# Kernel optimization log

Hardware: AMD Instinct MI355X
Metric: run time of the kernel (lower is better)

The kernel has to match this reference:

```python
import jax, jax.numpy as jnp
import numpy as np
from jax import lax

IMG, P, C, D, H, L, B = 256, 16, 3, 768, 12, 8, 2
G = IMG // P            # 16
N = G * G               # 256 patches
FF = 2048               # hard-coded FFN hidden dim in ViTBlockWithCCAttention
DH = D // H
EPS = 1e-5


def setup_inputs() -> dict:
    key = jax.random.key(0)
    ks = jax.random.split(key, 24)
    s = 0.02
    rn = lambda k, shp: jax.random.normal(k, shp, jnp.float32) * s
    inp = {
        "x": jax.random.normal(ks[0], (B, C, IMG, IMG), jnp.float32),
        "patch_w": rn(ks[1], (D, C * P * P)),
        "patch_b": rn(ks[2], (D,)),
        "pos_embed": rn(ks[3], (1, N, D)),
        # per-layer stacked params (shared nn.MultiheadAttention per block)
        "in_proj_w": rn(ks[4], (L, 3 * D, D)),
        "in_proj_b": rn(ks[5], (L, 3 * D)),
        "out_w": rn(ks[6], (L, D, D)),
        "out_b": rn(ks[7], (L, D)),
        "ln1_g": jnp.ones((L, D), jnp.float32),
        "ln1_b": jnp.zeros((L, D), jnp.float32),
        "ln2_g": jnp.ones((L, D), jnp.float32),
        "ln2_b": jnp.zeros((L, D), jnp.float32),
        "ffn_w1": rn(ks[8], (L, FF, D)),
        "ffn_b1": rn(ks[9], (L, FF)),
        "ffn_w2": rn(ks[10], (L, D, FF)),
        "ffn_b2": rn(ks[11], (L, D)),
        "edge_w": rn(ks[12], (D, 1)),
        "edge_b": rn(ks[13], (D,)),
        "conv1_w": rn(ks[14], (256, D, 3, 3)),
        "conv1_b": rn(ks[15], (256,)),
        "conv2_w": rn(ks[16], (1, 256, 1, 1)),
        "conv2_b": rn(ks[17], (1,)),
    }
    return inp


def _ln(z, g, b):
    m = z.mean(-1, keepdims=True)
    v = ((z - m) ** 2).mean(-1, keepdims=True)
    return (z - m) / jnp.sqrt(v + EPS) * g + b


def _mha(z, wi, bi, wo, bo):
    # z: (M, S, D). Returns out (M,S,D) and head-averaged attn weights (M,S,S)
    M, S, _ = z.shape
    qkv = z @ wi.T + bi
    q, k, v = jnp.split(qkv, 3, axis=-1)
    sp = lambda t: t.reshape(M, S, H, DH).transpose(0, 2, 1, 3)  # (M,H,S,dh)
    q, k, v = sp(q), sp(k), sp(v)
    a = jax.nn.softmax(jnp.einsum('mhqd,mhkd->mhqk', q, k) / np.sqrt(DH).astype(np.float32), axis=-1)
    o = jnp.einsum('mhqk,mhkd->mhqd', a, v).transpose(0, 2, 1, 3).reshape(M, S, D)
    return o @ wo.T + bo, a.mean(1)


def reference(x, patch_w, patch_b, pos_embed, in_proj_w, in_proj_b, out_w, out_b,
              ln1_g, ln1_b, ln2_g, ln2_b, ffn_w1, ffn_b1, ffn_w2, ffn_b2,
              edge_w, edge_b, conv1_w, conv1_b, conv2_w, conv2_b):
    Bc = x.shape[0]
    # patch embedding: unfold -> (B, N, C*P*P) -> linear
    patches = x.reshape(Bc, C, G, P, G, P).transpose(0, 2, 4, 1, 3, 5).reshape(Bc, N, C * P * P)
    h = patches @ patch_w.T + patch_b + pos_embed

    edge_sum = jnp.zeros((Bc, N, D), h.dtype)
    for i in range(L):
        xl = _ln(h, ln1_g[i], ln1_b[i])
        x2d = xl.reshape(Bc, G, G, D)
        # rows: sequences along height, one per column
        row_x = x2d.transpose(0, 2, 1, 3).reshape(Bc * G, G, D)
        row_out, row_a = _mha(row_x, in_proj_w[i], in_proj_b[i], out_w[i], out_b[i])
        # cols: sequences along width, one per row
        col_x = x2d.reshape(Bc * G, G, D)
        col_out, col_a = _mha(col_x, in_proj_w[i], in_proj_b[i], out_w[i], out_b[i])
        attn_out = (row_out.reshape(Bc, G, G, D).transpose(0, 2, 1, 3)
                    + col_out.reshape(Bc, G, G, D)).reshape(Bc, N, D)
        h = h + attn_out
        z = _ln(h, ln2_g[i], ln2_b[i])
        h = h + jax.nn.relu(z @ ffn_w1[i].T + ffn_b1[i]) @ ffn_w2[i].T + ffn_b2[i]
        # attention-divergence edge tokens (query-averaged attn maps)
        div = jnp.abs(row_a.mean(1) - col_a.mean(1)).reshape(Bc, N, 1)
        edge_sum = edge_sum + (div @ edge_w.T + edge_b)
    h = h + edge_sum / L

    feat = h.transpose(0, 2, 1).reshape(Bc, D, G, G)
    feat = jax.image.resize(feat, (Bc, D, IMG, IMG), method="bilinear")  # align_corners=False
    dn = ("NCHW", "OIHW", "NCHW")
    y = lax.conv_general_dilated(feat, conv1_w, (1, 1), "SAME", dimension_numbers=dn)
    y = jax.nn.relu(y + conv1_b[None, :, None, None])
    y = lax.conv_general_dilated(y, conv2_w, (1, 1), "SAME", dimension_numbers=dn)
    return y + conv2_b[None, :, None, None]
```

## Files before the change

kernel.cpp:

```cpp
#include <hip/hip_runtime.h>
#include <hip/hip_bf16.h>
#include <math.h>

#define BB 2
#define CIN 3
#define IMGS 256
#define PS 16
#define GG 16
#define NN 256
#define DIM 768
#define NH 12
#define NL 8
#define FFD 2048
#define LNEPS 1e-5f

typedef __attribute__((ext_vector_type(8))) short bf16x8;
typedef __attribute__((ext_vector_type(4))) float f32x4;

#define MB     1
#define MB2    2
#define MPOS   4
#define MRELU  8
#define MRES   16
#define MOBF16 32
#define MAS2   64
#define MBF32  128
#define MLNA   256
#define MAIM2  512

__device__ inline unsigned short bc(float f) {
    return __builtin_bit_cast(unsigned short, __float2bfloat16(f));
}

__device__ inline void gload16(const unsigned short* g, unsigned short* l) {
    __builtin_amdgcn_global_load_lds((const __attribute__((address_space(1))) void*)g,
                                     (__attribute__((address_space(3))) void*)l, 16, 0, 0);
}

template<int MODE, int BN>
__global__ __launch_bounds__(256) void gemm_bf16(
    const void* __restrict__ Av, const void* __restrict__ A2v, const void* __restrict__ Bv,
    const float* __restrict__ bias, const float* __restrict__ pos,
    const float2* __restrict__ stats, const float* __restrict__ lng,
    const float* __restrict__ lnb,
    float* __restrict__ C, unsigned short* __restrict__ C16,
    int M, int N, int K, int zdiv,
    long long sAo, long long sBi, long long sCo, long long sCi)
{
    constexpr int NI = BN / 32;
    int z = blockIdx.y;
    int zo = z / zdiv, zi = z % zdiv;
    const unsigned short* A16 = (const unsigned short*)Av + (size_t)zo * sAo;
    const float* Af  = (const float*)Av  + (size_t)zo * sAo;
    const float* Af2 = (const float*)A2v + (size_t)zo * sAo;
    const unsigned short* B16 = (const unsigned short*)Bv + (size_t)zi * sBi;
    const float* Bf  = (const float*)Bv  + (size_t)zi * sBi;
    long long coff = (long long)zo * sCo + (long long)zi * sCi;

    int NBY = M >> 5;
    int nbysh = 31 - __builtin_clz(NBY);
    int id = blockIdx.x;
    int qch = gridDim.x >> 3;
    int wgid = (id & 7) * qch + (id >> 3);
    int bx = wgid >> nbysh, by = wgid & (NBY - 1);
    int bm = by * 32, bn = bx * BN;

    __shared__ __align__(16) unsigned short As[2][2048], Bs[2][BN * 64];
    int tid = threadIdx.x;
    int lane = tid & 63, wave = tid >> 6;
    int wr = wave >> 1, wc = wave & 1;
    int sA = tid;
    int srowA = sA >> 3, schkA = (sA & 7) ^ (srowA & 7);

    f32x4 acc[NI] = {};
    f32x4 rA0, rA1, rA20, rA21, rB[NI][2], gv0, gv1, bv0, bv1;
    float2 strow;

    auto gstageA = [&](int b, int kt) {
        gload16(A16 + (size_t)(bm + srowA) * K + kt * 64 + schkA * 8, &As[b][sA * 8]);
    };
    auto gstageB = [&](int b, int kt) {
        #pragma unroll
        for (int i = 0; i < NI; ++i) {
            int s = tid + i * 256;
            int row = s >> 3, chk = (s & 7) ^ (row & 7);
            gload16(B16 + (size_t)(bn + row) * K + kt * 64 + chk * 8, &Bs[b][s * 8]);
        }
    };
    auto ldA = [&](int kt) {
        int k0 = kt * 64 + schkA * 8;
        if constexpr (MODE & MAIM2) {
            int m = bm + srowA;
            int bq = m >> 8, n = m & 255, gy = n >> 4, gx = n & 15;
            int c = k0 >> 8, rem = k0 & 255, py = rem >> 4, px = rem & 15;
            const float* src = Af + (((size_t)(bq * CIN + c) * IMGS + gy * PS + py) << 8)
                             + gx * PS + px;
            rA0 = *(const f32x4*)(src);
            rA1 = *(const f32x4*)(src + 4);
        } else {
            size_t off = (size_t)(bm + srowA) * K + k0;
            rA0 = *(const f32x4*)(Af + off);
            rA1 = *(const f32x4*)(Af + off + 4);
            if constexpr (MODE & MAS2) {
                rA20 = *(const f32x4*)(Af2 + off);
                rA21 = *(const f32x4*)(Af2 + off + 4);
            }
            if constexpr (MODE & MLNA) {
                strow = stats[bm + srowA];
                gv0 = *(const f32x4*)(lng + k0); gv1 = *(const f32x4*)(lng + k0 + 4);
                bv0 = *(const f32x4*)(lnb + k0); bv1 = *(const f32x4*)(lnb + k0 + 4);
            }
        }
    };
    auto ldB = [&](int kt) {
        #pragma unroll
        for (int i = 0; i < NI; ++i) {
            int s = tid + i * 256;
            int row = s >> 3, chk = (s & 7) ^ (row & 7);
            size_t off = (size_t)(bn + row) * K + kt * 64 + chk * 8;
            rB[i][0] = *(const f32x4*)(Bf + off);
            rB[i][1] = *(const f32x4*)(Bf + off + 4);
        }
    };
    auto wrA = [&](int b) {
        bf16x8 v;
        #pragma unroll
        for (int j = 0; j < 4; ++j) {
            float x0 = rA0[j], x1 = rA1[j];
            if constexpr (MODE & MAS2) { x0 += rA20[j]; x1 += rA21[j]; }
            if constexpr (MODE & MLNA) {
                x0 = (x0 - strow.x) * strow.y * gv0[j] + bv0[j];
                x1 = (x1 - strow.x) * strow.y * gv1[j] + bv1[j];
            }
            v[j] = (short)bc(x0); v[4 + j] = (short)bc(x1);
        }
        *(bf16x8*)(&As[b][sA * 8]) = v;
    };
    auto wrB = [&](int b) {
        #pragma unroll
        for (int i = 0; i < NI; ++i) {
            int s = tid + i * 256;
            bf16x8 v;
            #pragma unroll
            for (int j = 0; j < 4; ++j) {
                v[j] = (short)bc(rB[i][0][j]); v[4 + j] = (short)bc(rB[i][1][j]);
            }
            *(bf16x8*)(&Bs[b][s * 8]) = v;
        }
    };
    constexpr bool regA = (MODE & (MAS2 | MLNA | MAIM2)) != 0;
    auto compute = [&](int b) {
        const unsigned short* Ab = As[b];
        const unsigned short* Bb = Bs[b];
        int rl = lane & 15, kh = lane >> 4;
        #pragma unroll
        for (int ks = 0; ks < 2; ++ks) {
            int kc = ks * 4 + kh;
            int ar = 16 * wr + rl;
            bf16x8 af = *(const bf16x8*)(Ab + ar * 64 + (kc ^ (ar & 7)) * 8);
            #pragma unroll
            for (int ni = 0; ni < NI; ++ni) {
                int br = 16 * NI * wc + 16 * ni + rl;
                bf16x8 bf = *(const bf16x8*)(Bb + br * 64 + (kc ^ (br & 7)) * 8);
                acc[ni] = __builtin_amdgcn_mfma_f32_16x16x32_bf16(af, bf, acc[ni], 0, 0, 0);
            }
        }
    };

    int nt = K >> 6;
    if constexpr (!regA) gstageA(0, 0); else { ldA(0); wrA(0); }
    if constexpr (!(MODE & MBF32)) gstageB(0, 0); else { ldB(0); wrB(0); }
    __syncthreads();
    int buf = 0;
    for (int t = 0; t < nt; ++t) {
        if (t + 1 < nt) {
            if constexpr (!regA) gstageA(buf ^ 1, t + 1); else ldA(t + 1);
            if constexpr (!(MODE & MBF32)) gstageB(buf ^ 1, t + 1); else ldB(t + 1);
        }
        compute(buf);
        if (t + 1 < nt) {
            if constexpr (regA) wrA(buf ^ 1);
            if constexpr (MODE & MBF32) wrB(buf ^ 1);
        }
        __syncthreads();
        buf ^= 1;
    }

    #pragma unroll
    for (int ni = 0; ni < NI; ++ni) {
        #pragma unroll
        for (int r = 0; r < 4; ++r) {
            int row = bm + 16 * wr + (lane >> 4) * 4 + r;
            int col = bn + 16 * NI * wc + 16 * ni + (lane & 15);
            float v = acc[ni][r];
            if (MODE & (MB | MB2)) v += bias[col] * ((MODE & MB2) ? 2.f : 1.f);
            if (MODE & MPOS) v += pos[(size_t)(row & (NN - 1)) * N + col];
            if (MODE & MRELU) v = fmaxf(v, 0.f);
            long long ci = coff + (long long)row * N + col;
            if (MODE & MOBF16) C16[ci] = bc(v);
            else if (MODE & MRES) C[ci] += v;
            else C[ci] = v;
        }
    }
}

__global__ void wct_kernel(const float* __restrict__ w, unsigned short* __restrict__ Wct)
{
    int idx = blockIdx.x * 256 + threadIdx.x;
    int c = idx % DIM;
    int t = idx / DIM;
    int oc = t & 255;
    int dydx = t >> 8;
    int dy = dydx / 3, dx = dydx % 3;
    Wct[idx] = bc(w[((size_t)(oc * DIM + c) * 3 + dy) * 3 + dx]);
}

__global__ __launch_bounds__(256) void lnstat_kernel(const float* __restrict__ X,
                                                     float2* __restrict__ st)
{
    int row = blockIdx.x * 4 + (threadIdx.x >> 6);
    int lane = threadIdx.x & 63;
    const float* xp = X + (size_t)row * DIM + lane * 4;
    float s = 0.f, s2 = 0.f;
    #pragma unroll
    for (int seg = 0; seg < 3; ++seg) {
        f32x4 v = *(const f32x4*)(xp + seg * 256);
        s += v[0] + v[1] + v[2] + v[3];
        s2 += v[0] * v[0] + v[1] * v[1] + v[2] * v[2] + v[3] * v[3];
    }
    #pragma unroll
    for (int off = 32; off > 0; off >>= 1) {
        s  += __shfl_xor(s, off);
        s2 += __shfl_xor(s2, off);
    }
    if (lane == 0) {
        float mean = s * (1.f / DIM);
        float var = s2 * (1.f / DIM) - mean * mean;
        st[row] = make_float2(mean, rsqrtf(var + LNEPS));
    }
}

__global__ __launch_bounds__(256) void attn_kernel(
    const float* __restrict__ qkv, float* __restrict__ orow,
    float* __restrict__ ocol, float* __restrict__ amh)
{
    int b = blockIdx.x >> 4, g = blockIdx.x & 15;
    int type = blockIdx.y;
    int hh = blockIdx.z;
    int tid = threadIdx.x;
    __shared__ float qs[16][68], ks[16][68], vs[16][68], as_[16][17];
    {
        int sr = tid >> 4, dq = tid & 15;
        int n = (type == 0) ? (sr * GG + g) : (g * GG + sr);
        const float* base = qkv + (size_t)(b * NN + n) * (3 * DIM) + hh * 64 + dq * 4;
        float4 qv = *(const float4*)(base);
        float4 kv = *(const float4*)(base + DIM);
        float4 vv = *(const float4*)(base + 2 * DIM);
        *(float4*)&qs[sr][dq * 4] = qv;
        *(float4*)&ks[sr][dq * 4] = kv;
        *(float4*)&vs[sr][dq * 4] = vv;
    }
    __syncthreads();
    int s = tid >> 4, t = tid & 15;
    float sc = 0.f;
    #pragma unroll
    for (int d = 0; d < 64; ++d) sc += qs[s][d] * ks[t][d];
    sc *= 0.125f;
    float mx = sc;
    #pragma unroll
    for (int off = 1; off < 16; off <<= 1) mx = fmaxf(mx, __shfl_xor(mx, off, 16));
    float p = __expf(sc - mx);
    float sum = p;
    #pragma unroll
    for (int off = 1; off < 16; off <<= 1) sum += __shfl_xor(sum, off, 16);
    as_[s][t] = p / sum;
    __syncthreads();
    if (tid < 16) {
        float a = 0.f;
        #pragma unroll
        for (int ss = 0; ss < 16; ++ss) a += as_[ss][tid];
        amh[((size_t)(type * BB + b) * NN + g * GG + tid) * NH + hh] = a;
    }
    int s2 = tid >> 4, dg = (tid & 15) * 4;
    float o0 = 0, o1 = 0, o2 = 0, o3 = 0;
    #pragma unroll
    for (int t2 = 0; t2 < 16; ++t2) {
        float a2 = as_[s2][t2];
        o0 += a2 * vs[t2][dg];
        o1 += a2 * vs[t2][dg + 1];
        o2 += a2 * vs[t2][dg + 2];
        o3 += a2 * vs[t2][dg + 3];
    }
    int n2 = (type == 0) ? (s2 * GG + g) : (g * GG + s2);
    float* op = ((type == 0) ? orow : ocol) + (size_t)(b * NN + n2) * DIM + hh * 64 + dg;
    *(float4*)op = make_float4(o0, o1, o2, o3);
}

__global__ __launch_bounds__(256) void hfin_kernel(
    const float* __restrict__ h, const float* __restrict__ amh,
    const float* __restrict__ ew, const float* __restrict__ eb,
    unsigned short* __restrict__ hf)
{
    int m = blockIdx.x;
    int b = m >> 8, n = m & 255;
    int tid = threadIdx.x;
    __shared__ float divs;
    if (tid < 8) {
        const float* base = amh + (size_t)tid * 12288 + (size_t)b * 3072 + n * 12;
        float rs = 0.f, cs = 0.f;
        #pragma unroll
        for (int hh = 0; hh < NH; ++hh) {
            rs += base[hh];
            cs += base[6144 + hh];
        }
        float d = fabsf(rs - cs);
        d += __shfl_xor(d, 1);
        d += __shfl_xor(d, 2);
        d += __shfl_xor(d, 4);
        if (tid == 0) divs = d * (1.f / (NH * GG)) * (1.f / NL);
    }
    __syncthreads();
    float dv = divs;
    const float* hp = h + (size_t)m * DIM;
    unsigned short* yp = hf + (size_t)m * DIM;
    #pragma unroll
    for (int seg = 0; seg < 3; ++seg) {
        int d0 = tid + seg * 256;
        yp[d0] = bc(hp[d0] + dv * ew[d0] + eb[d0]);
    }
}

__global__ __launch_bounds__(256) void s_kernel(const float* __restrict__ P, float* __restrict__ S)
{
    int bdy = blockIdx.y;
    int b = bdy / 3, dy = bdy % 3;
    int ocg = blockIdx.x;
    __shared__ float Pl[3][4][16][17];
    int tid = threadIdx.x;
    #pragma unroll
    for (int l = 0; l < 12; ++l) {
        int e = l * 256 + tid;
        int dx = e >> 10, rem = e & 1023;
        int oc = rem >> 8, pix = rem & 255;
        int i = pix >> 4, j = pix & 15;
        Pl[dx][oc][j][i] =
            P[(((size_t)b * 9 + dy * 3 + dx) * 256 + ocg * 4 + oc) * 256 + pix];
    }
    __syncthreads();
    int xq = tid >> 6, oc = (tid >> 4) & 3, i = tid & 15;
    for (int xx = 0; xx < 64; ++xx) {
        int x = xq * 64 + xx;
        float acc = 0.f;
        #pragma unroll
        for (int dx = 0; dx < 3; ++dx) {
            int u = x + dx - 1;
            float p = (u + 0.5f) * 0.0625f - 0.5f;
            float fl = floorf(p);
            float f = p - fl;
            int j0 = (int)fl;
            int ja = j0 < 0 ? 0 : j0;
            int jb = (j0 + 1 > 15) ? 15 : (j0 + 1);
            bool valid = (u >= 0) && (u <= 255);
            float w0 = valid ? 1.f - f : 0.f;
            float w1 = valid ? f : 0.f;
            acc += w0 * Pl[dx][oc][ja][i] + w1 * Pl[dx][oc][jb][i];
        }
        S[(((size_t)(b * 256 + x) * 3 + dy) * 256 + ocg * 4 + oc) * 16 + i] = acc;
    }
}

__global__ __launch_bounds__(256) void out_kernel(
    const float* __restrict__ S, const float* __restrict__ b1,
    const float* __restrict__ w2, const float* __restrict__ b2p,
    float* __restrict__ out)
{
    int b = blockIdx.x >> 8, x = blockIdx.x & 255;
    __shared__ float Sl[12288];
    const float* Sp = S + (size_t)(b * 256 + x) * 12288;
    for (int l = threadIdx.x; l < 12288; l += 256) Sl[l] = Sp[l];
    __syncthreads();
    int y = threadIdx.x;
    float wy[3][2];
    int iy[3][2];
    #pragma unroll
    for (int dy = 0; dy < 3; ++dy) {
        int v = y + dy - 1;
        if (v < 0 || v > 255) {
            wy[dy][0] = wy[dy][1] = 0.f;
            iy[dy][0] = iy[dy][1] = 0;
        } else {
            float pp = (v + 0.5f) * 0.0625f - 0.5f;
            float fl = floorf(pp);
            float f = pp - fl;
            int i0 = (int)fl;
            iy[dy][0] = i0 < 0 ? 0 : i0;
            iy[dy][1] = (i0 + 1 > 15) ? 15 : (i0 + 1);
            wy[dy][0] = 1.f - f;
            wy[dy][1] = f;
        }
    }
    float acc = 0.f;
    for (int oc = 0; oc < 256; ++oc) {
        float sv = 0.f;
        #pragma unroll
        for (int dy = 0; dy < 3; ++dy)
            sv += wy[dy][0] * Sl[dy * 4096 + oc * 16 + iy[dy][0]]
                + wy[dy][1] * Sl[dy * 4096 + oc * 16 + iy[dy][1]];
        sv += b1[oc];
        acc += fmaxf(sv, 0.f) * w2[oc];
    }
    out[(size_t)b * 65536 + y * 256 + x] = acc + b2p[0];
}

extern "C" void kernel_launch(void* const* d_in, const int* in_sizes, int n_in,
                              void* d_out, int out_size, void* d_ws, size_t ws_size,
                              hipStream_t stream)
{
    const float* x         = (const float*)d_in[0];
    const float* patch_w   = (const float*)d_in[1];
    const float* patch_b   = (const float*)d_in[2];
    const float* pos_embed = (const float*)d_in[3];
    const float* in_proj_w = (const float*)d_in[4];
    const float* in_proj_b = (const float*)d_in[5];
    const float* out_w     = (const float*)d_in[6];
    const float* out_b     = (const float*)d_in[7];
    const float* ln1_g     = (const float*)d_in[8];
    const float* ln1_b     = (const float*)d_in[9];
    const float* ln2_g     = (const float*)d_in[10];
    const float* ln2_b     = (const float*)d_in[11];
    const float* ffn_w1    = (const float*)d_in[12];
    const float* ffn_b1    = (const float*)d_in[13];
    const float* ffn_w2    = (const float*)d_in[14];
    const float* ffn_b2    = (const float*)d_in[15];
    const float* edge_w    = (const float*)d_in[16];
    const float* edge_b    = (const float*)d_in[17];
    const float* conv1_w   = (const float*)d_in[18];
    const float* conv1_b   = (const float*)d_in[19];
    const float* conv2_w   = (const float*)d_in[20];
    const float* conv2_b   = (const float*)d_in[21];
    float* out = (float*)d_out;
    float* ws = (float*)d_ws;

    float* h      = ws;
    float* qkv    = h + 393216;
    float* orow   = qkv + 1179648;
    float* ocol   = orow + 393216;
    float* Pb     = ocol + 393216;
    float* Sb     = Pb + 1179648;
    float* amh    = Sb + 6291456;
    float2* stats = (float2*)(amh + 98304);
    unsigned short* hid16  = (unsigned short*)(amh + 98304 + 1024);
    unsigned short* hfin16 = hid16 + 1048576;
    unsigned short* Wct16  = hfin16 + 393216;

    wct_kernel<<<dim3(6912), 256, 0, stream>>>(conv1_w, Wct16);
    gemm_bf16<MB | MPOS | MAIM2 | MBF32, 32><<<dim3(24 * 16), 256, 0, stream>>>(
        x, nullptr, patch_w, patch_b, pos_embed, nullptr, nullptr, nullptr,
        h, nullptr, 512, 768, 768, 1, 0, 0, 0, 0);

    for (int l = 0; l < NL; ++l) {
        lnstat_kernel<<<dim3(128), 256, 0, stream>>>(h, stats);
        gemm_bf16<MB | MLNA | MBF32, 64><<<dim3(36 * 16), 256, 0, stream>>>(
            h, nullptr, in_proj_w + (size_t)l * 1769472,
            in_proj_b + (size_t)l * 2304, nullptr, stats,
            ln1_g + l * DIM, ln1_b + l * DIM, qkv, nullptr,
            512, 2304, 768, 1, 0, 0, 0, 0);
        attn_kernel<<<dim3(BB * GG, 2, NH), 256, 0, stream>>>(
            qkv, orow, ocol, amh + (size_t)l * 12288);
        gemm_bf16<MB2 | MRES | MAS2 | MBF32, 32><<<dim3(24 * 16), 256, 0, stream>>>(
            orow, ocol, out_w + (size_t)l * 589824,
            out_b + (size_t)l * DIM, nullptr, nullptr, nullptr, nullptr,
            h, nullptr, 512, 768, 768, 1, 0, 0, 0, 0);
        lnstat_kernel<<<dim3(128), 256, 0, stream>>>(h, stats);
        gemm_bf16<MB | MRELU | MOBF16 | MLNA | MBF32, 64><<<dim3(32 * 16), 256, 0, stream>>>(
            h, nullptr, ffn_w1 + (size_t)l * 1572864,
            ffn_b1 + (size_t)l * FFD, nullptr, stats,
            ln2_g + l * DIM, ln2_b + l * DIM, nullptr, hid16,
            512, 2048, 768, 1, 0, 0, 0, 0);
        gemm_bf16<MB | MRES | MBF32, 32><<<dim3(24 * 16), 256, 0, stream>>>(
            hid16, nullptr, ffn_w2 + (size_t)l * 1572864,
            ffn_b2 + (size_t)l * DIM, nullptr, nullptr, nullptr, nullptr,
            h, nullptr, 512, 768, 2048, 1, 0, 0, 0, 0);
    }

    hfin_kernel<<<dim3(512), 256, 0, stream>>>(h, amh, edge_w, edge_b, hfin16);
    gemm_bf16<0, 32><<<dim3(8 * 8, 18), 256, 0, stream>>>(
        Wct16, nullptr, hfin16, nullptr, nullptr, nullptr, nullptr, nullptr,
        Pb, nullptr, 256, 256, 768,
        2, 196608LL, 196608LL, 65536LL, 589824LL);
    s_kernel<<<dim3(64, 6), 256, 0, stream>>>(Pb, Sb);
    out_kernel<<<dim3(512), 256, 0, stream>>>(Sb, conv1_b, conv2_w, conv2_b, out);
}
```

Baseline: 663.7 us.

## Fuse LayerNorm stats into GEMM prologue and store conv intermediate as bf16

Removes the separate lnstat kernel launches: each LN-consuming GEMM block computes mean and rstd for its 32 rows into shared memory before the main loop. The intermediate S buffer between s_kernel and out_kernel is stored in bf16 instead of fp32, halving that traffic, and out_kernel unpacks it with vectorized loads. This trades 16 launches for redundant per-block stat computation (every column block recomputes the same rows) and adds bf16 rounding error on the conv intermediate.

```diff
diff --git a/kernel.cpp b/kernel.cpp
--- a/kernel.cpp
+++ b/kernel.cpp
@@ -15,6 +15,7 @@
 #define LNEPS 1e-5f
 
 typedef __attribute__((ext_vector_type(8))) short bf16x8;
+typedef __attribute__((ext_vector_type(8))) unsigned short u16x8;
 typedef __attribute__((ext_vector_type(4))) float f32x4;
 
 #define MB     1
@@ -31,6 +32,10 @@
 __device__ inline unsigned short bc(float f) {
     return __builtin_bit_cast(unsigned short, __float2bfloat16(f));
 }
+__device__ inline float fbc(unsigned short u) {
+    unsigned int x = ((unsigned int)u) << 16;
+    return __builtin_bit_cast(float, x);
+}
 
 __device__ inline void gload16(const unsigned short* g, unsigned short* l) {
     __builtin_amdgcn_global_load_lds((const __attribute__((address_space(1))) void*)g,
@@ -41,8 +46,7 @@
 __global__ __launch_bounds__(256) void gemm_bf16(
     const void* __restrict__ Av, const void* __restrict__ A2v, const void* __restrict__ Bv,
     const float* __restrict__ bias, const float* __restrict__ pos,
-    const float2* __restrict__ stats, const float* __restrict__ lng,
-    const float* __restrict__ lnb,
+    const float* __restrict__ lng, const float* __restrict__ lnb,
     float* __restrict__ C, unsigned short* __restrict__ C16,
     int M, int N, int K, int zdiv,
     long long sAo, long long sBi, long long sCo, long long sCi)
@@ -66,11 +70,35 @@
     int bm = by * 32, bn = bx * BN;
 
     __shared__ __align__(16) unsigned short As[2][2048], Bs[2][BN * 64];
+    __shared__ float2 sstat[32];
     int tid = threadIdx.x;
     int lane = tid & 63, wave = tid >> 6;
     int wr = wave >> 1, wc = wave & 1;
     int sA = tid;
     int srowA = sA >> 3, schkA = (sA & 7) ^ (srowA & 7);
+
+    if constexpr (MODE & MLNA) {
+        int r = tid >> 3, sub = tid & 7;
+        const float* rp = Af + (size_t)(bm + r) * K + sub * 96;
+        float s = 0.f, s2 = 0.f;
+        #pragma unroll
+        for (int i = 0; i < 24; ++i) {
+            f32x4 v = *(const f32x4*)(rp + i * 4);
+            s  += v[0] + v[1] + v[2] + v[3];
+            s2 += v[0]*v[0] + v[1]*v[1] + v[2]*v[2] + v[3]*v[3];
+        }
+        #pragma unroll
+        for (int m2 = 1; m2 < 8; m2 <<= 1) {
+            s  += __shfl_xor(s, m2);
+            s2 += __shfl_xor(s2, m2);
+        }
+        if (sub == 0) {
+            float mean = s * (1.f / DIM);
+            float var = s2 * (1.f / DIM) - mean * mean;
+            sstat[r] = make_float2(mean, rsqrtf(var + LNEPS));
+        }
+        __syncthreads();
+    }
 
     f32x4 acc[NI] = {};
     f32x4 rA0, rA1, rA20, rA21, rB[NI][2], gv0, gv1, bv0, bv1;
@@ -106,7 +134,7 @@
                 rA21 = *(const f32x4*)(Af2 + off + 4);
             }
             if constexpr (MODE & MLNA) {
-                strow = stats[bm + srowA];
+                strow = sstat[srowA];
                 gv0 = *(const f32x4*)(lng + k0); gv1 = *(const f32x4*)(lng + k0 + 4);
                 bv0 = *(const f32x4*)(lnb + k0); bv1 = *(const f32x4*)(lnb + k0 + 4);
             }
@@ -213,31 +241,6 @@
     int dydx = t >> 8;
     int dy = dydx / 3, dx = dydx % 3;
     Wct[idx] = bc(w[((size_t)(oc * DIM + c) * 3 + dy) * 3 + dx]);
-}
-
-__global__ __launch_bounds__(256) void lnstat_kernel(const float* __restrict__ X,
-                                                     float2* __restrict__ st)
-{
-    int row = blockIdx.x * 4 + (threadIdx.x >> 6);
-    int lane = threadIdx.x & 63;
-    const float* xp = X + (size_t)row * DIM + lane * 4;
-    float s = 0.f, s2 = 0.f;
-    #pragma unroll
-    for (int seg = 0; seg < 3; ++seg) {
-        f32x4 v = *(const f32x4*)(xp + seg * 256);
-        s += v[0] + v[1] + v[2] + v[3];
-        s2 += v[0] * v[0] + v[1] * v[1] + v[2] * v[2] + v[3] * v[3];
-    }
-    #pragma unroll
-    for (int off = 32; off > 0; off >>= 1) {
-        s  += __shfl_xor(s, off);
-        s2 += __shfl_xor(s2, off);
-    }
-    if (lane == 0) {
-        float mean = s * (1.f / DIM);
-        float var = s2 * (1.f / DIM) - mean * mean;
-        st[row] = make_float2(mean, rsqrtf(var + LNEPS));
-    }
 }
 
 __global__ __launch_bounds__(256) void attn_kernel(
@@ -330,7 +333,8 @@
     }
 }
 
-__global__ __launch_bounds__(256) void s_kernel(const float* __restrict__ P, float* __restrict__ S)
+__global__ __launch_bounds__(256) void s_kernel(const float* __restrict__ P,
+                                               unsigned short* __restrict__ S16)
 {
     int bdy = blockIdx.y;
     int b = bdy / 3, dy = bdy % 3;
@@ -365,19 +369,25 @@
             float w1 = valid ? f : 0.f;
             acc += w0 * Pl[dx][oc][ja][i] + w1 * Pl[dx][oc][jb][i];
         }
-        S[(((size_t)(b * 256 + x) * 3 + dy) * 256 + ocg * 4 + oc) * 16 + i] = acc;
+        S16[(((size_t)(b * 256 + x) * 3 + dy) * 256 + ocg * 4 + oc) * 16 + i] = bc(acc);
     }
 }
 
 __global__ __launch_bounds__(256) void out_kernel(
-    const float* __restrict__ S, const float* __restrict__ b1,
+    const unsigned short* __restrict__ S16, const float* __restrict__ b1,
     const float* __restrict__ w2, const float* __restrict__ b2p,
     float* __restrict__ out)
 {
     int b = blockIdx.x >> 8, x = blockIdx.x & 255;
     __shared__ float Sl[12288];
-    const float* Sp = S + (size_t)(b * 256 + x) * 12288;
-    for (int l = threadIdx.x; l < 12288; l += 256) Sl[l] = Sp[l];
+    const unsigned short* Sp = S16 + (size_t)(b * 256 + x) * 12288;
+    #pragma unroll
+    for (int c = 0; c < 6; ++c) {
+        int l8 = (c * 256 + threadIdx.x) * 8;
+        u16x8 v = *(const u16x8*)(Sp + l8);
+        #pragma unroll
+        for (int j = 0; j < 8; ++j) Sl[l8 + j] = fbc(v[j]);
+    }
     __syncthreads();
     int y = threadIdx.x;
     float wy[3][2];
@@ -446,48 +456,45 @@
     float* orow   = qkv + 1179648;
     float* ocol   = orow + 393216;
     float* Pb     = ocol + 393216;
-    float* Sb     = Pb + 1179648;
-    float* amh    = Sb + 6291456;
-    float2* stats = (float2*)(amh + 98304);
-    unsigned short* hid16  = (unsigned short*)(amh + 98304 + 1024);
+    float* amh    = Pb + 1179648;
+    unsigned short* Sb16   = (unsigned short*)(amh + 98304);
+    unsigned short* hid16  = Sb16 + 6291456;
     unsigned short* hfin16 = hid16 + 1048576;
     unsigned short* Wct16  = hfin16 + 393216;
 
     wct_kernel<<<dim3(6912), 256, 0, stream>>>(conv1_w, Wct16);
     gemm_bf16<MB | MPOS | MAIM2 | MBF32, 32><<<dim3(24 * 16), 256, 0, stream>>>(
-        x, nullptr, patch_w, patch_b, pos_embed, nullptr, nullptr, nullptr,
+        x, nullptr, patch_w, patch_b, pos_embed, nullptr, nullptr,
         h, nullptr, 512, 768, 768, 1, 0, 0, 0, 0);
 
     for (int l = 0; l < NL; ++l) {
-        lnstat_kernel<<<dim3(128), 256, 0, stream>>>(h, stats);
         gemm_bf16<MB | MLNA | MBF32, 64><<<dim3(36 * 16), 256, 0, stream>>>(
             h, nullptr, in_proj_w + (size_t)l * 1769472,
-            in_proj_b + (size_t)l * 2304, nullptr, stats,
+            in_proj_b + (size_t)l * 2304, nullptr,
             ln1_g + l * DIM, ln1_b + l * DIM, qkv, nullptr,
             512, 2304, 768, 1, 0, 0, 0, 0);
         attn_kernel<<<dim3(BB * GG, 2, NH), 256, 0, stream>>>(
             qkv, orow, ocol, amh + (size_t)l * 12288);
         gemm_bf16<MB2 | MRES | MAS2 | MBF32, 32><<<dim3(24 * 16), 256, 0, stream>>>(
             orow, ocol, out_w + (size_t)l * 589824,
-            out_b + (size_t)l * DIM, nullptr, nullptr, nullptr, nullptr,
+            out_b + (size_t)l * DIM, nullptr, nullptr, nullptr,
             h, nullptr, 512, 768, 768, 1, 0, 0, 0, 0);
-        lnstat_kernel<<<dim3(128), 256, 0, stream>>>(h, stats);
         gemm_bf16<MB | MRELU | MOBF16 | MLNA | MBF32, 64><<<dim3(32 * 16), 256, 0, stream>>>(
             h, nullptr, ffn_w1 + (size_t)l * 1572864,
-            ffn_b1 + (size_t)l * FFD, nullptr, stats,
+            ffn_b1 + (size_t)l * FFD, nullptr,
             ln2_g + l * DIM, ln2_b + l * DIM, nullptr, hid16,
             512, 2048, 768, 1, 0, 0, 0, 0);
         gemm_bf16<MB | MRES | MBF32, 32><<<dim3(24 * 16), 256, 0, stream>>>(
             hid16, nullptr, ffn_w2 + (size_t)l * 1572864,
-            ffn_b2 + (size_t)l * DIM, nullptr, nullptr, nullptr, nullptr,
+            ffn_b2 + (size_t)l * DIM, nullptr, nullptr, nullptr,
             h, nullptr, 512, 768, 2048, 1, 0, 0, 0, 0);
     }
 
     hfin_kernel<<<dim3(512), 256, 0, stream>>>(h, amh, edge_w, edge_b, hfin16);
     gemm_bf16<0, 32><<<dim3(8 * 8, 18), 256, 0, stream>>>(
-        Wct16, nullptr, hfin16, nullptr, nullptr, nullptr, nullptr, nullptr,
+        Wct16, nullptr, hfin16, nullptr, nullptr, nullptr, nullptr,
         Pb, nullptr, 256, 256, 768,
         2, 196608LL, 196608LL, 65536LL, 589824LL);
-    s_kernel<<<dim3(64, 6), 256, 0, stream>>>(Pb, Sb);
-    out_kernel<<<dim3(512), 256, 0, stream>>>(Sb, conv1_b, conv2_w, conv2_b, out);
-}
+    s_kernel<<<dim3(64, 6), 256, 0, stream>>>(Pb, Sb16);
+    out_kernel<<<dim3(512), 256, 0, stream>>>(Sb16, conv1_b, conv2_w, conv2_b, out);
+}
```

Result: slower. 690.0 us (+3.9%).

## Pre-convert all layer weights to bf16 and store S intermediate in bf16

Applied to the files above, without the earlier changes.

Adds conversion kernels that turn the fp32 patch and per-layer weights into bf16 once at the start, or layer by layer when the workspace is too small. The GEMMs then always stage B through direct global-to-LDS loads and drop the register-path fp32 convert. The S intermediate between s_kernel and out_kernel is also stored as bf16 to halve that traffic. The one-time conversion pass over roughly 88MB of fp32 weights is extra work inside the timed region, and bf16 storage of S reduces precision.

```diff
diff --git a/kernel.cpp b/kernel.cpp
--- a/kernel.cpp
+++ b/kernel.cpp
@@ -15,6 +15,7 @@
 #define LNEPS 1e-5f
 
 typedef __attribute__((ext_vector_type(8))) short bf16x8;
+typedef __attribute__((ext_vector_type(8))) unsigned short u16x8;
 typedef __attribute__((ext_vector_type(4))) float f32x4;
 
 #define MB     1
@@ -24,12 +25,21 @@
 #define MRES   16
 #define MOBF16 32
 #define MAS2   64
-#define MBF32  128
 #define MLNA   256
 #define MAIM2  512
 
+#define LW_IPW  0
+#define LW_OUTW 1769472
+#define LW_FW1  2359296
+#define LW_FW2  3932160
+#define LW_TOT  5505024
+
 __device__ inline unsigned short bc(float f) {
     return __builtin_bit_cast(unsigned short, __float2bfloat16(f));
+}
+__device__ inline float fbc(unsigned short u) {
+    unsigned int x = ((unsigned int)u) << 16;
+    return __builtin_bit_cast(float, x);
 }
 
 __device__ inline void gload16(const unsigned short* g, unsigned short* l) {
@@ -39,10 +49,11 @@
 
 template<int MODE, int BN>
 __global__ __launch_bounds__(256) void gemm_bf16(
-    const void* __restrict__ Av, const void* __restrict__ A2v, const void* __restrict__ Bv,
+    const void* __restrict__ Av, const void* __restrict__ A2v,
+    const unsigned short* __restrict__ B16,
     const float* __restrict__ bias, const float* __restrict__ pos,
-    const float2* __restrict__ stats, const float* __restrict__ lng,
-    const float* __restrict__ lnb,
+    const float2* __restrict__ stats,
+    const float* __restrict__ lng, const float* __restrict__ lnb,
     float* __restrict__ C, unsigned short* __restrict__ C16,
     int M, int N, int K, int zdiv,
     long long sAo, long long sBi, long long sCo, long long sCi)
@@ -53,8 +64,7 @@
     const unsigned short* A16 = (const unsigned short*)Av + (size_t)zo * sAo;
     const float* Af  = (const float*)Av  + (size_t)zo * sAo;
     const float* Af2 = (const float*)A2v + (size_t)zo * sAo;
-    const unsigned short* B16 = (const unsigned short*)Bv + (size_t)zi * sBi;
-    const float* Bf  = (const float*)Bv  + (size_t)zi * sBi;
+    B16 += (size_t)zi * sBi;
     long long coff = (long long)zo * sCo + (long long)zi * sCi;
 
     int NBY = M >> 5;
@@ -73,7 +83,7 @@
     int srowA = sA >> 3, schkA = (sA & 7) ^ (srowA & 7);
 
     f32x4 acc[NI] = {};
-    f32x4 rA0, rA1, rA20, rA21, rB[NI][2], gv0, gv1, bv0, bv1;
+    f32x4 rA0, rA1, rA20, rA21, gv0, gv1, bv0, bv1;
     float2 strow;
 
     auto gstageA = [&](int b, int kt) {
@@ -112,16 +122,6 @@
             }
         }
     };
-    auto ldB = [&](int kt) {
-        #pragma unroll
-        for (int i = 0; i < NI; ++i) {
-            int s = tid + i * 256;
-            int row = s >> 3, chk = (s & 7) ^ (row & 7);
-            size_t off = (size_t)(bn + row) * K + kt * 64 + chk * 8;
-            rB[i][0] = *(const f32x4*)(Bf + off);
-            rB[i][1] = *(const f32x4*)(Bf + off + 4);
-        }
-    };
     auto wrA = [&](int b) {
         bf16x8 v;
         #pragma unroll
@@ -135,18 +135,6 @@
             v[j] = (short)bc(x0); v[4 + j] = (short)bc(x1);
         }
         *(bf16x8*)(&As[b][sA * 8]) = v;
-    };
-    auto wrB = [&](int b) {
-        #pragma unroll
-        for (int i = 0; i < NI; ++i) {
-            int s = tid + i * 256;
-            bf16x8 v;
-            #pragma unroll
-            for (int j = 0; j < 4; ++j) {
-                v[j] = (short)bc(rB[i][0][j]); v[4 + j] = (short)bc(rB[i][1][j]);
-            }
-            *(bf16x8*)(&Bs[b][s * 8]) = v;
-        }
     };
     constexpr bool regA = (MODE & (MAS2 | MLNA | MAIM2)) != 0;
     auto compute = [&](int b) {
@@ -169,18 +157,17 @@
 
     int nt = K >> 6;
     if constexpr (!regA) gstageA(0, 0); else { ldA(0); wrA(0); }
-    if constexpr (!(MODE & MBF32)) gstageB(0, 0); else { ldB(0); wrB(0); }
+    gstageB(0, 0);
     __syncthreads();
     int buf = 0;
     for (int t = 0; t < nt; ++t) {
         if (t + 1 < nt) {
             if constexpr (!regA) gstageA(buf ^ 1, t + 1); else ldA(t + 1);
-            if constexpr (!(MODE & MBF32)) gstageB(buf ^ 1, t + 1); else ldB(t + 1);
+            gstageB(buf ^ 1, t + 1);
         }
         compute(buf);
         if (t + 1 < nt) {
             if constexpr (regA) wrA(buf ^ 1);
-            if constexpr (MODE & MBF32) wrB(buf ^ 1);
         }
         __syncthreads();
         buf ^= 1;
@@ -213,6 +200,45 @@
     int dydx = t >> 8;
     int dy = dydx / 3, dx = dydx % 3;
     Wct[idx] = bc(w[((size_t)(oc * DIM + c) * 3 + dy) * 3 + dx]);
+}
+
+__global__ void cvt4_kernel(const float* __restrict__ src, unsigned short* __restrict__ dst, int n4)
+{
+    int i4 = blockIdx.x * 256 + threadIdx.x;
+    if (i4 >= n4) return;
+    f32x4 v = *(const f32x4*)(src + i4 * 4);
+    int i = i4 * 4;
+    dst[i] = bc(v[0]); dst[i + 1] = bc(v[1]); dst[i + 2] = bc(v[2]); dst[i + 3] = bc(v[3]);
+}
+
+__global__ void cvtall_kernel(const float* __restrict__ ipw, const float* __restrict__ ow,
+                              const float* __restrict__ f1, const float* __restrict__ f2,
+                              unsigned short* __restrict__ dst)
+{
+    long long i = (long long)(blockIdx.x * 256 + threadIdx.x) * 4;
+    int l = (int)(i / LW_TOT);
+    int r = (int)(i - (long long)l * LW_TOT);
+    const float* src; long long off;
+    if (r < LW_OUTW)      { src = ipw; off = (long long)l * 1769472 + r; }
+    else if (r < LW_FW1)  { src = ow;  off = (long long)l * 589824 + (r - LW_OUTW); }
+    else if (r < LW_FW2)  { src = f1;  off = (long long)l * 1572864 + (r - LW_FW1); }
+    else                  { src = f2;  off = (long long)l * 1572864 + (r - LW_FW2); }
+    f32x4 v = *(const f32x4*)(src + off);
+    dst[i] = bc(v[0]); dst[i + 1] = bc(v[1]); dst[i + 2] = bc(v[2]); dst[i + 3] = bc(v[3]);
+}
+
+__global__ void cvtlayer_kernel(const float* __restrict__ ipw, const float* __restrict__ ow,
+                                const float* __restrict__ f1, const float* __restrict__ f2,
+                                unsigned short* __restrict__ dst)
+{
+    int i = (blockIdx.x * 256 + threadIdx.x) * 4;
+    const float* src; int off;
+    if (i < LW_OUTW)      { src = ipw; off = i; }
+    else if (i < LW_FW1)  { src = ow;  off = i - LW_OUTW; }
+    else if (i < LW_FW2)  { src = f1;  off = i - LW_FW1; }
+    else                  { src = f2;  off = i - LW_FW2; }
+    f32x4 v = *(const f32x4*)(src + off);
+    dst[i] = bc(v[0]); dst[i + 1] = bc(v[1]); dst[i + 2] = bc(v[2]); dst[i + 3] = bc(v[3]);
 }
 
 __global__ __launch_bounds__(256) void lnstat_kernel(const float* __restrict__ X,
@@ -330,7 +356,8 @@
     }
 }
 
-__global__ __launch_bounds__(256) void s_kernel(const float* __restrict__ P, float* __restrict__ S)
+__global__ __launch_bounds__(256) void s_kernel(const float* __restrict__ P,
+                                               unsigned short* __restrict__ S16)
 {
     int bdy = blockIdx.y;
     int b = bdy / 3, dy = bdy % 3;
@@ -365,19 +392,25 @@
             float w1 = valid ? f : 0.f;
             acc += w0 * Pl[dx][oc][ja][i] + w1 * Pl[dx][oc][jb][i];
         }
-        S[(((size_t)(b * 256 + x) * 3 + dy) * 256 + ocg * 4 + oc) * 16 + i] = acc;
+        S16[(((size_t)(b * 256 + x) * 3 + dy) * 256 + ocg * 4 + oc) * 16 + i] = bc(acc);
     }
 }
 
 __global__ __launch_bounds__(256) void out_kernel(
-    const float* __restrict__ S, const float* __restrict__ b1,
+    const unsigned short* __restrict__ S16, const float* __restrict__ b1,
     const float* __restrict__ w2, const float* __restrict__ b2p,
     float* __restrict__ out)
 {
     int b = blockIdx.x >> 8, x = blockIdx.x & 255;
     __shared__ float Sl[12288];
-    const float* Sp = S + (size_t)(b * 256 + x) * 12288;
-    for (int l = threadIdx.x; l < 12288; l += 256) Sl[l] = Sp[l];
+    const unsigned short* Sp = S16 + (size_t)(b * 256 + x) * 12288;
+    #pragma unroll
+    for (int c = 0; c < 6; ++c) {
+        int l8 = (c * 256 + threadIdx.x) * 8;
+        u16x8 v = *(const u16x8*)(Sp + l8);
+        #pragma unroll
+        for (int j = 0; j < 8; ++j) Sl[l8 + j] = fbc(v[j]);
+    }
     __syncthreads();
     int y = threadIdx.x;
     float wy[3][2];
@@ -446,41 +479,55 @@
     float* orow   = qkv + 1179648;
     float* ocol   = orow + 393216;
     float* Pb     = ocol + 393216;
-    float* Sb     = Pb + 1179648;
-    float* amh    = Sb + 6291456;
+    float* amh    = Pb + 1179648;
     float2* stats = (float2*)(amh + 98304);
-    unsigned short* hid16  = (unsigned short*)(amh + 98304 + 1024);
+    unsigned short* Sb16   = (unsigned short*)(stats + 512);
+    unsigned short* hid16  = Sb16 + 6291456;
     unsigned short* hfin16 = hid16 + 1048576;
     unsigned short* Wct16  = hfin16 + 393216;
+    unsigned short* pw16   = Wct16 + 1769472;
+    unsigned short* lw16   = pw16 + 589824;
+
+    size_t base_shorts = 6291456 + 1048576 + 393216 + 1769472 + 589824;
+    size_t base_bytes = (size_t)(393216 + 1179648 + 393216 + 393216 + 1179648 + 98304 + 1024) * 4
+                      + base_shorts * 2;
+    bool big = ws_size >= base_bytes + (size_t)8 * LW_TOT * 2;
 
     wct_kernel<<<dim3(6912), 256, 0, stream>>>(conv1_w, Wct16);
-    gemm_bf16<MB | MPOS | MAIM2 | MBF32, 32><<<dim3(24 * 16), 256, 0, stream>>>(
-        x, nullptr, patch_w, patch_b, pos_embed, nullptr, nullptr, nullptr,
+    cvt4_kernel<<<dim3(576), 256, 0, stream>>>(patch_w, pw16, 147456);
+    if (big)
+        cvtall_kernel<<<dim3(43008), 256, 0, stream>>>(in_proj_w, out_w, ffn_w1, ffn_w2, lw16);
+
+    gemm_bf16<MB | MPOS | MAIM2, 32><<<dim3(24 * 16), 256, 0, stream>>>(
+        x, nullptr, pw16, patch_b, pos_embed, nullptr, nullptr, nullptr,
         h, nullptr, 512, 768, 768, 1, 0, 0, 0, 0);
 
     for (int l = 0; l < NL; ++l) {
+        const unsigned short* lw = big ? lw16 + (size_t)l * LW_TOT : lw16;
+        if (!big)
+            cvtlayer_kernel<<<dim3(5376), 256, 0, stream>>>(
+                in_proj_w + (size_t)l * 1769472, out_w + (size_t)l * 589824,
+                ffn_w1 + (size_t)l * 1572864, ffn_w2 + (size_t)l * 1572864, lw16);
         lnstat_kernel<<<dim3(128), 256, 0, stream>>>(h, stats);
-        gemm_bf16<MB | MLNA | MBF32, 64><<<dim3(36 * 16), 256, 0, stream>>>(
-            h, nullptr, in_proj_w + (size_t)l * 1769472,
-            in_proj_b + (size_t)l * 2304, nullptr, stats,
-            ln1_g + l * DIM, ln1_b + l * DIM, qkv, nullptr,
+        gemm_bf16<MB | MLNA, 64><<<dim3(36 * 16), 256, 0, stream>>>(
+            h, nullptr, lw + LW_IPW, in_proj_b + (size_t)l * 2304, nullptr,
+            stats, ln1_g + l * DIM, ln1_b + l * DIM, qkv, nullptr,
             512, 2304, 768, 1, 0, 0, 0, 0);
         attn_kernel<<<dim3(BB * GG, 2, NH), 256, 0, stream>>>(
             qkv, orow, ocol, amh + (size_t)l * 12288);
-        gemm_bf16<MB2 | MRES | MAS2 | MBF32, 32><<<dim3(24 * 16), 256, 0, stream>>>(
-            orow, ocol, out_w + (size_t)l * 589824,
-            out_b + (size_t)l * DIM, nullptr, nullptr, nullptr, nullptr,
-            h, nullptr, 512, 768, 768, 1, 0, 0, 0, 0);
+        gemm_bf16<MB2 | MRES | MAS2, 32><<<dim3(24 * 16), 256, 0, stream>>>(
+            orow, ocol, lw + LW_OUTW, out_b + (size_t)l * DIM, nullptr,
+            nullptr, nullptr, nullptr, h, nullptr,
+            512, 768, 768, 1, 0, 0, 0, 0);
         lnstat_kernel<<<dim3(128), 256, 0, stream>>>(h, stats);
-        gemm_bf16<MB | MRELU | MOBF16 | MLNA | MBF32, 64><<<dim3(32 * 16), 256, 0, stream>>>(
-            h, nullptr, ffn_w1 + (size_t)l * 1572864,
-            ffn_b1 + (size_t)l * FFD, nullptr, stats,
-            ln2_g + l * DIM, ln2_b + l * DIM, nullptr, hid16,
+        gemm_bf16<MB | MRELU | MOBF16 | MLNA, 64><<<dim3(32 * 16), 256, 0, stream>>>(
+            h, nullptr, lw + LW_FW1, ffn_b1 + (size_t)l * FFD, nullptr,
+            stats, ln2_g + l * DIM, ln2_b + l * DIM, nullptr, hid16,
             512, 2048, 768, 1, 0, 0, 0, 0);
-        gemm_bf16<MB | MRES | MBF32, 32><<<dim3(24 * 16), 256, 0, stream>>>(
-            hid16, nullptr, ffn_w2 + (size_t)l * 1572864,
-            ffn_b2 + (size_t)l * DIM, nullptr, nullptr, nullptr, nullptr,
-            h, nullptr, 512, 768, 2048, 1, 0, 0, 0, 0);
+        gemm_bf16<MB | MRES, 32><<<dim3(24 * 16), 256, 0, stream>>>(
+            hid16, nullptr, lw + LW_FW2, ffn_b2 + (size_t)l * DIM, nullptr,
+            nullptr, nullptr, nullptr, h, nullptr,
+            512, 768, 2048, 1, 0, 0, 0, 0);
     }
 
     hfin_kernel<<<dim3(512), 256, 0, stream>>>(h, amh, edge_w, edge_b, hfin16);
@@ -488,6 +535,6 @@
         Wct16, nullptr, hfin16, nullptr, nullptr, nullptr, nullptr, nullptr,
         Pb, nullptr, 256, 256, 768,
         2, 196608LL, 196608LL, 65536LL, 589824LL);
-    s_kernel<<<dim3(64, 6), 256, 0, stream>>>(Pb, Sb);
-    out_kernel<<<dim3(512), 256, 0, stream>>>(Sb, conv1_b, conv2_w, conv2_b, out);
-}
+    s_kernel<<<dim3(64, 6), 256, 0, stream>>>(Pb, Sb16);
+    out_kernel<<<dim3(512), 256, 0, stream>>>(Sb16, conv1_b, conv2_w, conv2_b, out);
+}
```

Result: no change. 662.5 us (-0.2%).
